# Kernel tuning notes

Hardware: AMD Instinct MI355X
Metric: run time of the kernel (lower is better)

Reference implementation:

```python
import jax, jax.numpy as jnp
import numpy as np

FP16_HUGE = 2.0 ** 15
NUM_HEAD = 4
LN_EPS = 1e-5


def setup_inputs() -> dict:
    key = jax.random.key(0)
    ks = jax.random.split(key, 12)
    B, N, D = 1, 256, 128
    H = NUM_HEAD
    inp = {
        "pair_act": jax.random.normal(ks[0], (B, N, N, D), dtype=jnp.float32),
        "pair_mask": jnp.ones((B, N, N), dtype=jnp.float32),
        "ln_scale": jnp.ones((D,), dtype=jnp.float32),
        "ln_bias": jnp.zeros((D,), dtype=jnp.float32),
        # torch Linear weight layout: [out_dim, in_dim]; applied as x @ W.T
        "w2d": jax.random.normal(ks[1], (H, D), dtype=jnp.float32) / np.sqrt(D),
        "wq": jax.random.normal(ks[2], (D, D), dtype=jnp.float32) / np.sqrt(D),
        "wk": jax.random.normal(ks[3], (D, D), dtype=jnp.float32) / np.sqrt(D),
        "wv": jax.random.normal(ks[4], (D, D), dtype=jnp.float32) / np.sqrt(D),
        "wg": jax.random.normal(ks[5], (D, D), dtype=jnp.float32) / np.sqrt(D),
        "bg": jnp.ones((D,), dtype=jnp.float32),  # gating bias init = 1.0
        "wo": jax.random.normal(ks[6], (D, D), dtype=jnp.float32) * 0.02,
        "bo": jnp.zeros((D,), dtype=jnp.float32),
    }
    return inp


def reference(pair_act, pair_mask, ln_scale, ln_bias, w2d, wq, wk, wv, wg, bg, wo, bo):
    B, N, _, D = pair_act.shape
    H = NUM_HEAD
    kd = D // H  # per-head key/value dim
    scale = kd ** (-0.5)

    # mask bias: [B, N(row), 1, 1, N(key)]
    bias = (FP16_HUGE * (pair_mask - 1.0))[:, :, None, None, :]

    # LayerNorm (fp32, eps=1e-5)
    mu = jnp.mean(pair_act, axis=-1, keepdims=True)
    var = jnp.mean(jnp.square(pair_act - mu), axis=-1, keepdims=True)
    x = (pair_act - mu) * jax.lax.rsqrt(var + LN_EPS) * ln_scale + ln_bias

    # non-batched per-head bias: [B, 1, H, N, N]
    nb = jnp.einsum("bijd,hd->bhij", x, w2d)[:, None]

    q = (x @ wq.T).reshape(B, N, N, H, kd) * scale  # [B, r, i, H, kd]
    k = (x @ wk.T).reshape(B, N, N, H, kd)
    v = (x @ wv.T).reshape(B, N, N, H, kd)

    logits = jnp.einsum("brihk,brjhk->brhij", q, k) + bias + nb  # [B, r, H, i, j]
    w = jax.nn.softmax(logits, axis=-1)
    o = jnp.einsum("brhij,brjhv->brihv", w, v)  # [B, r, i, H, kd]

    g = jax.nn.sigmoid(x @ wg.T + bg).reshape(B, N, N, H, kd)
    o = (o * g).reshape(B, N, N, D)

    out = o @ wo.T + bo
    return out * pair_mask[..., None]
```

## Files before the change

### kernel.cpp

```cpp
#include <hip/hip_runtime.h>
#include <hip/hip_bf16.h>

typedef unsigned short u16;
typedef __attribute__((ext_vector_type(8))) short bf16x8;
typedef __attribute__((ext_vector_type(4))) float f32x4;

#define N 256
#define D 128
#define NH 4
#define KD 32
#define NN 65536
#define QK_SCALE 0.17677669529663687f
#define HUGE_MASK 32768.0f

__device__ __forceinline__ float b2f(u16 s) {
  union { float f; unsigned u; } x; x.u = ((unsigned)s) << 16; return x.f;
}
__device__ __forceinline__ u16 f2b(float f) {
  union { float f; unsigned u; } x; x.f = f;
  unsigned r = x.u + 0x7fff + ((x.u >> 16) & 1);
  return (u16)(r >> 16);
}

__device__ __forceinline__ void stage_w(const float* __restrict__ W, u16* Wlds, int tid) {
  int row = tid >> 1, cb = (tid & 1) * 64;
#pragma unroll
  for (int j = 0; j < 8; j++) {
    float4 f0 = *(const float4*)(W + row * 128 + cb + j * 8);
    float4 f1 = *(const float4*)(W + row * 128 + cb + j * 8 + 4);
    uint4 pk;
    pk.x = (unsigned)f2b(f0.x) | ((unsigned)f2b(f0.y) << 16);
    pk.y = (unsigned)f2b(f0.z) | ((unsigned)f2b(f0.w) << 16);
    pk.z = (unsigned)f2b(f1.x) | ((unsigned)f2b(f1.y) << 16);
    pk.w = (unsigned)f2b(f1.z) | ((unsigned)f2b(f1.w) << 16);
    int g = (cb >> 3) + j;
    int gp = (g + (row & 15)) & 15;
    *(uint4*)(&Wlds[row * 128 + gp * 8]) = pk;
  }
}

__global__ __launch_bounds__(256) void projln_kernel(
    const float* __restrict__ pa, const float* __restrict__ lns, const float* __restrict__ lnb,
    const float* __restrict__ w2d,
    const float* __restrict__ wq, const float* __restrict__ wk,
    const float* __restrict__ wv, const float* __restrict__ wg,
    const float* __restrict__ bg,
    u16* __restrict__ q, u16* __restrict__ k, u16* __restrict__ v, u16* __restrict__ g,
    float* __restrict__ nbT)
{
  __shared__ __align__(16) u16 Wlds[128 * 128];
  int tid = threadIdx.x;
  int wave = tid >> 6, lane = tid & 63;
  int lr = lane & 15, quad = lane >> 4;

  bf16x8 a[2][4];
#pragma unroll
  for (int mt = 0; mt < 2; mt++) {
    int row = blockIdx.x * 128 + wave * 32 + mt * 16 + lr;
    const float* rp = pa + (size_t)row * D;
    float xv[4][8];
    float s = 0.f, ss = 0.f;
#pragma unroll
    for (int ks = 0; ks < 4; ks++) {
      float4 a0 = *(const float4*)(rp + ks * 32 + quad * 8);
      float4 a1 = *(const float4*)(rp + ks * 32 + quad * 8 + 4);
      xv[ks][0] = a0.x; xv[ks][1] = a0.y; xv[ks][2] = a0.z; xv[ks][3] = a0.w;
      xv[ks][4] = a1.x; xv[ks][5] = a1.y; xv[ks][6] = a1.z; xv[ks][7] = a1.w;
#pragma unroll
      for (int j = 0; j < 8; j++) { s += xv[ks][j]; ss += xv[ks][j] * xv[ks][j]; }
    }
    s  += __shfl_xor(s, 16, 64);  ss += __shfl_xor(ss, 16, 64);
    s  += __shfl_xor(s, 32, 64);  ss += __shfl_xor(ss, 32, 64);
    float mu = s * (1.0f / D);
    float var = ss * (1.0f / D) - mu * mu;
    float rs = rsqrtf(var + 1e-5f);
#pragma unroll
    for (int ks = 0; ks < 4; ks++) {
      float4 s0 = *(const float4*)(lns + ks * 32 + quad * 8);
      float4 s1 = *(const float4*)(lns + ks * 32 + quad * 8 + 4);
      float4 b0 = *(const float4*)(lnb + ks * 32 + quad * 8);
      float4 b1 = *(const float4*)(lnb + ks * 32 + quad * 8 + 4);
      float sc[8] = {s0.x,s0.y,s0.z,s0.w,s1.x,s1.y,s1.z,s1.w};
      float bi[8] = {b0.x,b0.y,b0.z,b0.w,b1.x,b1.y,b1.z,b1.w};
#pragma unroll
      for (int j = 0; j < 8; j++) xv[ks][j] = (xv[ks][j] - mu) * rs * sc[j] + bi[j];
    }
#pragma unroll
    for (int h = 0; h < NH; h++) {
      float p = 0.f;
#pragma unroll
      for (int ks = 0; ks < 4; ks++) {
        float4 w0 = *(const float4*)(w2d + h * D + ks * 32 + quad * 8);
        float4 w1 = *(const float4*)(w2d + h * D + ks * 32 + quad * 8 + 4);
        p += xv[ks][0]*w0.x + xv[ks][1]*w0.y + xv[ks][2]*w0.z + xv[ks][3]*w0.w
           + xv[ks][4]*w1.x + xv[ks][5]*w1.y + xv[ks][6]*w1.z + xv[ks][7]*w1.w;
      }
      p += __shfl_xor(p, 16, 64);
      p += __shfl_xor(p, 32, 64);
      if (quad == 0)
        nbT[(size_t)h * NN + (size_t)(row & 255) * 256 + (row >> 8)] = p;
    }
#pragma unroll
    for (int ks = 0; ks < 4; ks++)
#pragma unroll
      for (int j = 0; j < 8; j++) a[mt][ks][j] = (short)f2b(xv[ks][j]);
  }

  const float* Ws[4] = {wq, wk, wv, wg};
  u16* Os[4] = {q, k, v, g};
#pragma unroll
  for (int mat = 0; mat < 4; mat++) {
    stage_w(Ws[mat], Wlds, tid);
    __syncthreads();
    f32x4 acc[2][2][4];
#pragma unroll
    for (int mt = 0; mt < 2; mt++)
#pragma unroll
      for (int tg = 0; tg < 2; tg++)
#pragma unroll
        for (int e = 0; e < 4; e++) acc[mt][tg][e] = (f32x4){0.f, 0.f, 0.f, 0.f};
#pragma unroll
    for (int ks = 0; ks < 4; ks++) {
#pragma unroll
      for (int tg = 0; tg < 2; tg++) {
#pragma unroll
        for (int e = 0; e < 4; e++) {
          int nrow = tg * 64 + 4 * lr + e;
          int gp = (ks * 4 + quad + (nrow & 15)) & 15;
          bf16x8 b = *(const bf16x8*)(&Wlds[nrow * 128 + gp * 8]);
          acc[0][tg][e] = __builtin_amdgcn_mfma_f32_16x16x32_bf16(a[0][ks], b, acc[0][tg][e], 0, 0, 0);
          acc[1][tg][e] = __builtin_amdgcn_mfma_f32_16x16x32_bf16(a[1][ks], b, acc[1][tg][e], 0, 0, 0);
        }
      }
    }
    u16* O = Os[mat];
#pragma unroll
    for (int mt = 0; mt < 2; mt++) {
      int row0 = blockIdx.x * 128 + wave * 32 + mt * 16 + quad * 4;
#pragma unroll
      for (int tg = 0; tg < 2; tg++) {
        int c0 = tg * 64 + 4 * lr;
        float bg0 = 0.f, bg1 = 0.f, bg2 = 0.f, bg3 = 0.f;
        if (mat == 3) { bg0 = bg[c0]; bg1 = bg[c0+1]; bg2 = bg[c0+2]; bg3 = bg[c0+3]; }
#pragma unroll
        for (int reg = 0; reg < 4; reg++) {
          float v0 = acc[mt][tg][0][reg], v1 = acc[mt][tg][1][reg];
          float v2 = acc[mt][tg][2][reg], v3 = acc[mt][tg][3][reg];
          if (mat == 0) { v0 *= QK_SCALE; v1 *= QK_SCALE; v2 *= QK_SCALE; v3 *= QK_SCALE; }
          if (mat == 3) {
            v0 = 1.0f / (1.0f + __expf(-(v0 + bg0)));
            v1 = 1.0f / (1.0f + __expf(-(v1 + bg1)));
            v2 = 1.0f / (1.0f + __expf(-(v2 + bg2)));
            v3 = 1.0f / (1.0f + __expf(-(v3 + bg3)));
          }
          uint2 pk;
          pk.x = (unsigned)f2b(v0) | ((unsigned)f2b(v1) << 16);
          pk.y = (unsigned)f2b(v2) | ((unsigned)f2b(v3) << 16);
          *(uint2*)(O + (size_t)(row0 + reg) * D + c0) = pk;
        }
      }
    }
    __syncthreads();
  }
}

__global__ __launch_bounds__(256) void attn_kernel(
    const u16* __restrict__ q, const u16* __restrict__ k, const u16* __restrict__ v,
    const u16* __restrict__ g, const float* __restrict__ nbT, const float* __restrict__ mask,
    u16* __restrict__ og)
{
  __shared__ __align__(16) u16 Kf[8192];
  __shared__ __align__(16) u16 Vf[8192];
  __shared__ __align__(16) u16 Pf[16384];
  __shared__ float bias_lds[256];
  int h = blockIdx.x & 3, r = blockIdx.x >> 2;
  int tid = threadIdx.x;
  {
    int j = tid;
    const u16* krow = k + ((size_t)r * N + j) * D + h * KD;
    int t = j >> 4, lrj = j & 15;
#pragma unroll
    for (int qc = 0; qc < 4; qc++)
      *(bf16x8*)(&Kf[((t * 4 + qc) * 16 + lrj) * 8]) = *(const bf16x8*)(krow + qc * 8);
    const u16* vrow = v + ((size_t)r * N + j) * D + h * KD;
    int ks = j >> 5, qj = (j >> 3) & 3, jj = j & 7;
#pragma unroll
    for (int c = 0; c < 32; c++)
      Vf[(((ks * 2 + (c & 1)) * 4 + qj) * 16 + (c >> 1)) * 8 + jj] = vrow[c];
    bias_lds[tid] = HUGE_MASK * (mask[r * N + tid] - 1.0f);
  }
  __syncthreads();
  int wave = tid >> 6, lane = tid & 63;
  int lr = lane & 15, quad = lane >> 4;
  u16* Pw = &Pf[wave * 4096];
  float bias_v[16];
#pragma unroll
  for (int t = 0; t < 16; t++) bias_v[t] = bias_lds[t * 16 + lr];
  const float* nbh = nbT + (size_t)h * NN;

  for (int pass = 0; pass < 4; pass++) {
    int i0 = pass * 64 + wave * 16;
    bf16x8 af = *(const bf16x8*)(q + ((size_t)r * N + i0 + lr) * D + h * KD + quad * 8);
    f32x4 S[16];
#pragma unroll
    for (int t = 0; t < 16; t++) {
      bf16x8 bfr = *(const bf16x8*)(&Kf[((t * 4 + quad) * 16 + lr) * 8]);
      S[t] = __builtin_amdgcn_mfma_f32_16x16x32_bf16(af, bfr, (f32x4){0.f,0.f,0.f,0.f}, 0, 0, 0);
    }
    float mx[4] = {-3e38f, -3e38f, -3e38f, -3e38f};
#pragma unroll
    for (int t = 0; t < 16; t++) {
      float4 nb4 = *(const float4*)(nbh + (size_t)(t * 16 + lr) * N + i0 + quad * 4);
      float bl = bias_v[t];
      S[t][0] += nb4.x + bl;  S[t][1] += nb4.y + bl;
      S[t][2] += nb4.z + bl;  S[t][3] += nb4.w + bl;
      mx[0] = fmaxf(mx[0], S[t][0]); mx[1] = fmaxf(mx[1], S[t][1]);
      mx[2] = fmaxf(mx[2], S[t][2]); mx[3] = fmaxf(mx[3], S[t][3]);
    }
#pragma unroll
    for (int reg = 0; reg < 4; reg++) {
#pragma unroll
      for (int off = 8; off; off >>= 1)
        mx[reg] = fmaxf(mx[reg], __shfl_xor(mx[reg], off, 16));
    }
    float lsum[4] = {0.f, 0.f, 0.f, 0.f};
#pragma unroll
    for (int t = 0; t < 16; t++) {
      int j = t * 16 + lr;
      int cbase = ((j >> 5) * 4 + ((j >> 3) & 3)) * 128 + (j & 7);
#pragma unroll
      for (int reg = 0; reg < 4; reg++) {
        float p = __expf(S[t][reg] - mx[reg]);
        lsum[reg] += p;
        union { float f; unsigned u; } cv; cv.f = p;
        Pw[cbase + (quad * 4 + reg) * 8] = (u16)((cv.u + 0x8000u) >> 16);
      }
    }
#pragma unroll
    for (int reg = 0; reg < 4; reg++) {
#pragma unroll
      for (int off = 8; off; off >>= 1)
        lsum[reg] += __shfl_xor(lsum[reg], off, 16);
    }
    __asm__ __volatile__("s_waitcnt lgkmcnt(0)" ::: "memory");
    f32x4 o[2] = {(f32x4){0.f,0.f,0.f,0.f}, (f32x4){0.f,0.f,0.f,0.f}};
#pragma unroll
    for (int ks = 0; ks < 8; ks++) {
      bf16x8 pa = *(const bf16x8*)(&Pw[((ks * 4 + quad) * 16 + lr) * 8]);
#pragma unroll
      for (int e = 0; e < 2; e++) {
        bf16x8 vb = *(const bf16x8*)(&Vf[(((ks * 2 + e) * 4 + quad) * 16 + lr) * 8]);
        o[e] = __builtin_amdgcn_mfma_f32_16x16x32_bf16(pa, vb, o[e], 0, 0, 0);
      }
    }
#pragma unroll
    for (int reg = 0; reg < 4; reg++) {
      float inv = __builtin_amdgcn_rcpf(lsum[reg]);
      int i = i0 + quad * 4 + reg;
      size_t base = ((size_t)r * N + i) * D + h * KD + 2 * lr;
      unsigned gv = *(const unsigned*)(g + base);
      float r0 = o[0][reg] * inv * b2f((u16)(gv & 0xffff));
      float r1 = o[1][reg] * inv * b2f((u16)(gv >> 16));
      *(unsigned*)(og + base) = (unsigned)f2b(r0) | ((unsigned)f2b(r1) << 16);
    }
  }
}

__global__ __launch_bounds__(256) void out_kernel(
    const u16* __restrict__ og, const float* __restrict__ wo, const float* __restrict__ bo,
    const float* __restrict__ mask, float* __restrict__ out)
{
  __shared__ __align__(16) u16 Wlds[128 * 128];
  int tid = threadIdx.x;
  stage_w(wo, Wlds, tid);
  int wave = tid >> 6, lane = tid & 63;
  int lr = lane & 15, quad = lane >> 4;
  bf16x8 a[2][4];
#pragma unroll
  for (int mt = 0; mt < 2; mt++) {
    int arow = blockIdx.x * 128 + wave * 32 + mt * 16 + lr;
#pragma unroll
    for (int ks = 0; ks < 4; ks++)
      a[mt][ks] = *(const bf16x8*)(og + (size_t)arow * D + ks * 32 + quad * 8);
  }
  __syncthreads();
  f32x4 acc[2][2][4];
#pragma unroll
  for (int mt = 0; mt < 2; mt++)
#pragma unroll
    for (int tg = 0; tg < 2; tg++)
#pragma unroll
      for (int e = 0; e < 4; e++) acc[mt][tg][e] = (f32x4){0.f, 0.f, 0.f, 0.f};
#pragma unroll
  for (int ks = 0; ks < 4; ks++) {
#pragma unroll
    for (int tg = 0; tg < 2; tg++) {
#pragma unroll
      for (int e = 0; e < 4; e++) {
        int nrow = tg * 64 + 4 * lr + e;
        int gp = (ks * 4 + quad + (nrow & 15)) & 15;
        bf16x8 b = *(const bf16x8*)(&Wlds[nrow * 128 + gp * 8]);
        acc[0][tg][e] = __builtin_amdgcn_mfma_f32_16x16x32_bf16(a[0][ks], b, acc[0][tg][e], 0, 0, 0);
        acc[1][tg][e] = __builtin_amdgcn_mfma_f32_16x16x32_bf16(a[1][ks], b, acc[1][tg][e], 0, 0, 0);
      }
    }
  }
#pragma unroll
  for (int mt = 0; mt < 2; mt++) {
    int row0 = blockIdx.x * 128 + wave * 32 + mt * 16 + quad * 4;
#pragma unroll
    for (int tg = 0; tg < 2; tg++) {
      int c0 = tg * 64 + 4 * lr;
      float4 bo4 = *(const float4*)(bo + c0);
#pragma unroll
      for (int reg = 0; reg < 4; reg++) {
        int pos = row0 + reg;
        float m = mask[pos];
        float4 o4;
        o4.x = (acc[mt][tg][0][reg] + bo4.x) * m;
        o4.y = (acc[mt][tg][1][reg] + bo4.y) * m;
        o4.z = (acc[mt][tg][2][reg] + bo4.z) * m;
        o4.w = (acc[mt][tg][3][reg] + bo4.w) * m;
        *(float4*)(out + (size_t)pos * D + c0) = o4;
      }
    }
  }
}

extern "C" void kernel_launch(void* const* d_in, const int* in_sizes, int n_in,
                              void* d_out, int out_size, void* d_ws, size_t ws_size,
                              hipStream_t stream)
{
  const float* pa   = (const float*)d_in[0];
  const float* mask = (const float*)d_in[1];
  const float* lns  = (const float*)d_in[2];
  const float* lnb  = (const float*)d_in[3];
  const float* w2d  = (const float*)d_in[4];
  const float* wq   = (const float*)d_in[5];
  const float* wk   = (const float*)d_in[6];
  const float* wv   = (const float*)d_in[7];
  const float* wg   = (const float*)d_in[8];
  const float* bg   = (const float*)d_in[9];
  const float* wo   = (const float*)d_in[10];
  const float* bo   = (const float*)d_in[11];

  const size_t ARR = (size_t)NN * D;
  u16* q  = (u16*)d_ws;
  u16* k  = q + ARR;
  u16* v  = k + ARR;
  u16* g  = v + ARR;
  u16* og = g + ARR;
  float* nbT = (float*)(og + ARR);

  projln_kernel<<<512, 256, 0, stream>>>(pa, lns, lnb, w2d, wq, wk, wv, wg, bg, q, k, v, g, nbT);
  attn_kernel<<<N * NH, 256, 0, stream>>>(q, k, v, g, nbT, mask, og);
  out_kernel<<<512, 256, 0, stream>>>(og, wo, bo, mask, (float*)d_out);
}
```

Baseline: 202.3 us.

## Pre-convert weights to swizzled bf16 and double-buffer async LDS staging

A new prep kernel converts the five fp32 weight matrices once into a bf16, pre-swizzled workspace buffer. The projection and output kernels then stage that buffer straight into LDS with global_load_lds, instead of each block converting fp32 weights itself. The projection kernel double-buffers the weights, prefetching the next matrix while running MFMAs on the current one. This removes repeated per-block conversion and overlaps weight staging with compute, at the cost of an extra kernel launch and reliance on barriers to order the async LDS writes.

Result: faster. 187.6 us (-7.3%).

```diff
diff --git a/kernel.cpp b/kernel.cpp
--- a/kernel.cpp
+++ b/kernel.cpp
@@ -4,6 +4,8 @@
 typedef unsigned short u16;
 typedef __attribute__((ext_vector_type(8))) short bf16x8;
 typedef __attribute__((ext_vector_type(4))) float f32x4;
+typedef __attribute__((address_space(3))) unsigned lds_u32;
+typedef const __attribute__((address_space(1))) unsigned glb_u32;
 
 #define N 256
 #define D 128
@@ -22,36 +24,50 @@
   return (u16)(r >> 16);
 }
 
-__device__ __forceinline__ void stage_w(const float* __restrict__ W, u16* Wlds, int tid) {
-  int row = tid >> 1, cb = (tid & 1) * 64;
-#pragma unroll
-  for (int j = 0; j < 8; j++) {
-    float4 f0 = *(const float4*)(W + row * 128 + cb + j * 8);
-    float4 f1 = *(const float4*)(W + row * 128 + cb + j * 8 + 4);
-    uint4 pk;
-    pk.x = (unsigned)f2b(f0.x) | ((unsigned)f2b(f0.y) << 16);
-    pk.y = (unsigned)f2b(f0.z) | ((unsigned)f2b(f0.w) << 16);
-    pk.z = (unsigned)f2b(f1.x) | ((unsigned)f2b(f1.y) << 16);
-    pk.w = (unsigned)f2b(f1.z) | ((unsigned)f2b(f1.w) << 16);
-    int g = (cb >> 3) + j;
-    int gp = (g + (row & 15)) & 15;
-    *(uint4*)(&Wlds[row * 128 + gp * 8]) = pk;
+__global__ __launch_bounds__(256) void prep_w_kernel(
+    const float* __restrict__ wq, const float* __restrict__ wk,
+    const float* __restrict__ wv, const float* __restrict__ wg,
+    const float* __restrict__ wo, u16* __restrict__ wb)
+{
+  int idx = blockIdx.x * 256 + threadIdx.x;
+  const float* srcs[5] = {wq, wk, wv, wg, wo};
+  int mat = idx >> 11, rem = idx & 2047;
+  int row = rem >> 4, g = rem & 15;
+  int gp = (g + (row & 15)) & 15;
+  const float* s = srcs[mat] + row * 128 + g * 8;
+  float4 f0 = *(const float4*)(s);
+  float4 f1 = *(const float4*)(s + 4);
+  uint4 pk;
+  pk.x = (unsigned)f2b(f0.x) | ((unsigned)f2b(f0.y) << 16);
+  pk.y = (unsigned)f2b(f0.z) | ((unsigned)f2b(f0.w) << 16);
+  pk.z = (unsigned)f2b(f1.x) | ((unsigned)f2b(f1.y) << 16);
+  pk.w = (unsigned)f2b(f1.z) | ((unsigned)f2b(f1.w) << 16);
+  *(uint4*)(wb + (size_t)mat * 16384 + row * 128 + gp * 8) = pk;
+}
+
+__device__ __forceinline__ void async_stage(const u16* __restrict__ gsrc, u16* lds, int tid) {
+  int lane = tid & 63, wave = tid >> 6;
+  u16* lbase = lds + wave * 512;
+  const u16* gbase = gsrc + wave * 512 + lane * 8;
+#pragma unroll
+  for (int p = 0; p < 8; p++) {
+    __builtin_amdgcn_global_load_lds((glb_u32*)(gbase + p * 2048),
+                                     (lds_u32*)(lbase + p * 2048), 16, 0, 0);
   }
 }
 
 __global__ __launch_bounds__(256) void projln_kernel(
     const float* __restrict__ pa, const float* __restrict__ lns, const float* __restrict__ lnb,
-    const float* __restrict__ w2d,
-    const float* __restrict__ wq, const float* __restrict__ wk,
-    const float* __restrict__ wv, const float* __restrict__ wg,
-    const float* __restrict__ bg,
+    const float* __restrict__ w2d, const u16* __restrict__ wb, const float* __restrict__ bg,
     u16* __restrict__ q, u16* __restrict__ k, u16* __restrict__ v, u16* __restrict__ g,
     float* __restrict__ nbT)
 {
-  __shared__ __align__(16) u16 Wlds[128 * 128];
+  __shared__ __align__(16) u16 Wl[2][16384];
   int tid = threadIdx.x;
   int wave = tid >> 6, lane = tid & 63;
   int lr = lane & 15, quad = lane >> 4;
+
+  async_stage(wb, Wl[0], tid);
 
   bf16x8 a[2][4];
 #pragma unroll
@@ -105,13 +121,13 @@
 #pragma unroll
       for (int j = 0; j < 8; j++) a[mt][ks][j] = (short)f2b(xv[ks][j]);
   }
-
-  const float* Ws[4] = {wq, wk, wv, wg};
+  __syncthreads();
+
   u16* Os[4] = {q, k, v, g};
 #pragma unroll
   for (int mat = 0; mat < 4; mat++) {
-    stage_w(Ws[mat], Wlds, tid);
-    __syncthreads();
+    if (mat < 3) async_stage(wb + (size_t)(mat + 1) * 16384, Wl[(mat + 1) & 1], tid);
+    const u16* Wcur = Wl[mat & 1];
     f32x4 acc[2][2][4];
 #pragma unroll
     for (int mt = 0; mt < 2; mt++)
@@ -127,7 +143,7 @@
         for (int e = 0; e < 4; e++) {
           int nrow = tg * 64 + 4 * lr + e;
           int gp = (ks * 4 + quad + (nrow & 15)) & 15;
-          bf16x8 b = *(const bf16x8*)(&Wlds[nrow * 128 + gp * 8]);
+          bf16x8 b = *(const bf16x8*)(&Wcur[nrow * 128 + gp * 8]);
           acc[0][tg][e] = __builtin_amdgcn_mfma_f32_16x16x32_bf16(a[0][ks], b, acc[0][tg][e], 0, 0, 0);
           acc[1][tg][e] = __builtin_amdgcn_mfma_f32_16x16x32_bf16(a[1][ks], b, acc[1][tg][e], 0, 0, 0);
         }
@@ -267,12 +283,12 @@
 }
 
 __global__ __launch_bounds__(256) void out_kernel(
-    const u16* __restrict__ og, const float* __restrict__ wo, const float* __restrict__ bo,
+    const u16* __restrict__ og, const u16* __restrict__ wob, const float* __restrict__ bo,
     const float* __restrict__ mask, float* __restrict__ out)
 {
-  __shared__ __align__(16) u16 Wlds[128 * 128];
+  __shared__ __align__(16) u16 Wlds[16384];
   int tid = threadIdx.x;
-  stage_w(wo, Wlds, tid);
+  async_stage(wob, Wlds, tid);
   int wave = tid >> 6, lane = tid & 63;
   int lr = lane & 15, quad = lane >> 4;
   bf16x8 a[2][4];
@@ -351,8 +367,10 @@
   u16* g  = v + ARR;
   u16* og = g + ARR;
   float* nbT = (float*)(og + ARR);
-
-  projln_kernel<<<512, 256, 0, stream>>>(pa, lns, lnb, w2d, wq, wk, wv, wg, bg, q, k, v, g, nbT);
+  u16* wb = (u16*)(nbT + (size_t)NH * NN);
+
+  prep_w_kernel<<<40, 256, 0, stream>>>(wq, wk, wv, wg, wo, wb);
+  projln_kernel<<<512, 256, 0, stream>>>(pa, lns, lnb, w2d, wb, bg, q, k, v, g, nbT);
   attn_kernel<<<N * NH, 256, 0, stream>>>(q, k, v, g, nbT, mask, og);
-  out_kernel<<<512, 256, 0, stream>>>(og, wo, bo, mask, (float*)d_out);
-}
+  out_kernel<<<512, 256, 0, stream>>>(og, wb + 4 * 16384, bo, mask, (float*)d_out);
+}
```
